# Optimization experiments

Hardware: AMD Instinct MI355X
Metric: run time of the kernel (lower is better)

## Reference

```python
import jax, jax.numpy as jnp
import numpy as np
import math

D = 512; NA = 128; NC = 256; NB = 128; BATCH = 4; H = 8
EA, EC, EB = 4, 6, 4
KA, KC, KB = 2, 1, 2
F = 4 * D  # expert_ff_mult * embed_dim
N_TOTAL = NA + NC + NB


def setup_inputs() -> dict:
    key = jax.random.key(0)
    ks = jax.random.split(key, 16)
    s = 0.02
    def nrm(k, shape, scale=s):
        return jax.random.normal(k, shape, dtype=jnp.float32) * scale
    return {
        'tokens_A': jax.random.normal(ks[0], (BATCH, NA, D), dtype=jnp.float32),
        'tokens_B': jax.random.normal(ks[1], (BATCH, NB, D), dtype=jnp.float32),
        'tokens_C': jax.random.normal(ks[2], (BATCH, NC, D), dtype=jnp.float32),
        'ln1_g': jnp.ones((3, D), jnp.float32), 'ln1_b': jnp.zeros((3, D), jnp.float32),
        'ln2_g': jnp.ones((3, D), jnp.float32), 'ln2_b': jnp.zeros((3, D), jnp.float32),
        'Wqkv': nrm(ks[3], (3 * D, D)), 'bqkv': jnp.zeros((3 * D,), jnp.float32),
        'Wo': nrm(ks[4], (D, D)), 'bo': jnp.zeros((D,), jnp.float32),
        'Wr_A': nrm(ks[5], (D, EA)), 'br_A': jnp.zeros((EA,), jnp.float32),
        'W1_A': nrm(ks[6], (EA, D, F)), 'b1_A': jnp.zeros((EA, F), jnp.float32),
        'W2_A': nrm(ks[7], (EA, F, D)), 'b2_A': jnp.zeros((EA, D), jnp.float32),
        'Wr_C': nrm(ks[8], (D, EC)), 'br_C': jnp.zeros((EC,), jnp.float32),
        'W1_C': nrm(ks[9], (EC, D, F)), 'b1_C': jnp.zeros((EC, F), jnp.float32),
        'W2_C': nrm(ks[10], (EC, F, D)), 'b2_C': jnp.zeros((EC, D), jnp.float32),
        'Wr_B': nrm(ks[11], (D, EB)), 'br_B': jnp.zeros((EB,), jnp.float32),
        'W1_B': nrm(ks[12], (EB, D, F)), 'b1_B': jnp.zeros((EB, F), jnp.float32),
        'W2_B': nrm(ks[13], (EB, F, D)), 'b2_B': jnp.zeros((EB, D), jnp.float32),
    }


def _ln(x, g, b, eps=1e-5):
    m = jnp.mean(x, axis=-1, keepdims=True)
    v = jnp.var(x, axis=-1, keepdims=True)
    return (x - m) * jax.lax.rsqrt(v + eps) * g + b


def _directed_mask_bias():
    # segments: 0=A, 1=C, 2=B in [A|C|B] order; query may attend upstream groups only
    seg = jnp.concatenate([jnp.zeros(NA), jnp.ones(NC), 2.0 * jnp.ones(NB)])
    allowed = seg[None, :] <= seg[:, None]  # (N, N)
    return jnp.where(allowed, 0.0, -1e9).astype(jnp.float32)


def _mha(x, Wqkv, bqkv, Wo, bo, mask_bias):
    B, N, _ = x.shape
    qkv = x @ Wqkv.T + bqkv  # (B, N, 3D)
    q, k, v = jnp.split(qkv, 3, axis=-1)
    hd = D // H
    def heads(t):
        return t.reshape(B, N, H, hd).transpose(0, 2, 1, 3)  # (B, H, N, hd)
    q, k, v = heads(q), heads(k), heads(v)
    scores = jnp.einsum('bhqd,bhkd->bhqk', q, k) / math.sqrt(hd) + mask_bias[None, None]
    attn = jax.nn.softmax(scores, axis=-1)
    o = jnp.einsum('bhqk,bhkd->bhqd', attn, v).transpose(0, 2, 1, 3).reshape(B, N, D)
    return o @ Wo.T + bo


def _moe(x, Wr, br, W1, b1, W2, b2, k):
    # top-k routed expert FFN: softmax gates -> top-k renormalized -> dense combine
    probs = jax.nn.softmax(x @ Wr + br, axis=-1)  # (B, N, E)
    vals, idx = jax.lax.top_k(probs, k)
    vals = vals / jnp.sum(vals, axis=-1, keepdims=True)
    E = Wr.shape[1]
    gate = jnp.sum(jax.nn.one_hot(idx, E, dtype=x.dtype) * vals[..., None], axis=-2)  # (B, N, E)
    h = jax.nn.gelu(jnp.einsum('bnd,edf->benf', x, W1) + b1[None, :, None, :])
    y = jnp.einsum('benf,efd->bend', h, W2) + b2[None, :, None, :]
    return jnp.einsum('bne,bend->bnd', gate, y)


def reference(tokens_A, tokens_B, tokens_C, ln1_g, ln1_b, ln2_g, ln2_b,
              Wqkv, bqkv, Wo, bo,
              Wr_A, br_A, W1_A, b1_A, W2_A, b2_A,
              Wr_C, br_C, W1_C, b1_C, W2_C, b2_C,
              Wr_B, br_B, W1_B, b1_B, W2_B, b2_B):
    # 1-2. group-local pre-attention LN, concat [A | C | B]
    x = jnp.concatenate([
        _ln(tokens_A, ln1_g[0], ln1_b[0]),
        _ln(tokens_C, ln1_g[1], ln1_b[1]),
        _ln(tokens_B, ln1_g[2], ln1_b[2]),
    ], axis=1)
    # 3-4. shared directed self-attention + per-group residual
    attn = _mha(x, Wqkv, bqkv, Wo, bo, _directed_mask_bias())
    tA = tokens_A + attn[:, :NA]
    tC = tokens_C + attn[:, NA:NA + NC]
    tB = tokens_B + attn[:, NA + NC:]
    # 5. group-local pre-expert LN
    nA = _ln(tA, ln2_g[0], ln2_b[0])
    nC = _ln(tC, ln2_g[1], ln2_b[1])
    nB = _ln(tB, ln2_g[2], ln2_b[2])
    # 6-9. route A and C first, then B; residual add per group
    tA = tA + _moe(nA, Wr_A, br_A, W1_A, b1_A, W2_A, b2_A, KA)
    tC = tC + _moe(nC, Wr_C, br_C, W1_C, b1_C, W2_C, b2_C, KC)
    tB = tB + _moe(nB, Wr_B, br_B, W1_B, b1_B, W2_B, b2_B, KB)
    return jnp.concatenate([tA, tC, tB], axis=1)  # (B, NA+NC+NB, D)
```

## Files before the change

### kernel.cpp

```cpp
#include <hip/hip_runtime.h>
#include <hip/hip_bf16.h>
#include <cstdint>

#define DEV __device__ __forceinline__

using f32x4  = __attribute__((ext_vector_type(4))) float;
using bf16x8 = __attribute__((ext_vector_type(8))) __bf16;

static constexpr int D_    = 512;
static constexpr int ROWS  = 2048;
static constexpr int F_    = 2048;
static constexpr int NEXP  = 14;
static constexpr int NENT  = 3072;

DEV unsigned short f2bf(float f) {
  unsigned int u = __builtin_bit_cast(unsigned int, f);
  unsigned int r = u + 0x7FFFu + ((u >> 16) & 1u);
  return (unsigned short)(r >> 16);
}
DEV unsigned int pack2(float a, float b) {
  return (unsigned int)f2bf(a) | ((unsigned int)f2bf(b) << 16);
}
DEV float gelu_tanh(float x) {
  float x3 = x * x * x;
  return 0.5f * x * (1.0f + tanhf(0.7978845608028654f * (x + 0.044715f * x3)));
}
DEV int prefix_base(const int* cnt, int e) {
  int base = 0;
  for (int i = 0; i < e; ++i) base += cnt[i];
  return base;
}

struct Shared128 { unsigned short As[128][72]; unsigned short Bs[64][72]; };

DEV void gemm128(const unsigned short* arow, const float* B, int ldb, int bcol0, int K,
                 f32x4 (&acc)[2][4], Shared128& sh)
{
  const int tid = threadIdx.x;
  const int lane = tid & 63, w = tid >> 6;
  const int ai = tid >> 1, ah = tid & 1;
  const int bj = tid >> 2, bq = tid & 3;
  for (int k0 = 0; k0 < K; k0 += 64) {
    __syncthreads();
    {
      const uint4* src = reinterpret_cast<const uint4*>(arow + k0 + ah * 32);
      uint4 v0 = src[0], v1 = src[1], v2 = src[2], v3 = src[3];
      uint4* dst = reinterpret_cast<uint4*>(&sh.As[ai][ah * 32]);
      dst[0] = v0; dst[1] = v1; dst[2] = v2; dst[3] = v3;
    }
    {
      const float4* src = reinterpret_cast<const float4*>(B + (size_t)(bcol0 + bj) * ldb + k0 + bq * 16);
      unsigned int pk[8];
      #pragma unroll
      for (int u = 0; u < 4; ++u) {
        float4 f = src[u];
        pk[u * 2]     = pack2(f.x, f.y);
        pk[u * 2 + 1] = pack2(f.z, f.w);
      }
      uint4* dst = reinterpret_cast<uint4*>(&sh.Bs[bj][bq * 16]);
      dst[0] = make_uint4(pk[0], pk[1], pk[2], pk[3]);
      dst[1] = make_uint4(pk[4], pk[5], pk[6], pk[7]);
    }
    __syncthreads();
    #pragma unroll
    for (int ks = 0; ks < 2; ++ks) {
      bf16x8 a[2], b[4];
      #pragma unroll
      for (int mi = 0; mi < 2; ++mi)
        a[mi] = *reinterpret_cast<const bf16x8*>(&sh.As[w * 32 + mi * 16 + (lane & 15)][ks * 32 + (lane >> 4) * 8]);
      #pragma unroll
      for (int ni = 0; ni < 4; ++ni)
        b[ni] = *reinterpret_cast<const bf16x8*>(&sh.Bs[ni * 16 + (lane & 15)][ks * 32 + (lane >> 4) * 8]);
      #pragma unroll
      for (int mi = 0; mi < 2; ++mi)
        #pragma unroll
        for (int ni = 0; ni < 4; ++ni)
          acc[mi][ni] = __builtin_amdgcn_mfma_f32_16x16x32_bf16(a[mi], b[ni], acc[mi][ni], 0, 0, 0);
    }
  }
}

struct Shared64x128 { unsigned short As[64][72]; unsigned short Bs[128][72]; };

DEV void gemm64x128(const unsigned short* arow, const unsigned short* B, int ldb, int bcol0, int K,
                    f32x4 (&acc)[8], Shared64x128& sh)
{
  const int tid = threadIdx.x;
  const int lane = tid & 63, w = tid >> 6;
  const int ar = tid >> 2, aq = tid & 3;
  const int br = tid >> 1, bh = tid & 1;
  for (int k0 = 0; k0 < K; k0 += 64) {
    __syncthreads();
    {
      const uint4* srcA = reinterpret_cast<const uint4*>(arow + k0 + aq * 16);
      uint4 a0 = srcA[0], a1 = srcA[1];
      uint4* dstA = reinterpret_cast<uint4*>(&sh.As[ar][aq * 16]);
      dstA[0] = a0; dstA[1] = a1;
      const uint4* srcB = reinterpret_cast<const uint4*>(B + (size_t)(bcol0 + br) * ldb + k0 + bh * 32);
      uint4 b0 = srcB[0], b1 = srcB[1], b2 = srcB[2], b3 = srcB[3];
      uint4* dstB = reinterpret_cast<uint4*>(&sh.Bs[br][bh * 32]);
      dstB[0] = b0; dstB[1] = b1; dstB[2] = b2; dstB[3] = b3;
    }
    __syncthreads();
    #pragma unroll
    for (int ks = 0; ks < 2; ++ks) {
      bf16x8 a = *reinterpret_cast<const bf16x8*>(&sh.As[w * 16 + (lane & 15)][ks * 32 + (lane >> 4) * 8]);
      #pragma unroll
      for (int ni = 0; ni < 8; ++ni) {
        bf16x8 b = *reinterpret_cast<const bf16x8*>(&sh.Bs[ni * 16 + (lane & 15)][ks * 32 + (lane >> 4) * 8]);
        acc[ni] = __builtin_amdgcn_mfma_f32_16x16x32_bf16(a, b, acc[ni], 0, 0, 0);
      }
    }
  }
}

__global__ __launch_bounds__(256) void k_ln(
    const float* tA, const float* tC, const float* tB,
    const float* g3, const float* b3, unsigned short* out)
{
  int r = blockIdx.x;
  int b = r >> 9, n = r & 511;
  int grp = n < 128 ? 0 : (n < 384 ? 1 : 2);
  const float* src = grp == 0 ? tA + (size_t)(b * 128 + n) * D_
                   : grp == 1 ? tC + (size_t)(b * 256 + n - 128) * D_
                              : tB + (size_t)(b * 128 + n - 384) * D_;
  int tid = threadIdx.x, lane = tid & 63, w = tid >> 6;
  float2 v = *reinterpret_cast<const float2*>(src + tid * 2);
  float s = v.x + v.y;
  float ss = v.x * v.x + v.y * v.y;
  #pragma unroll
  for (int off = 1; off < 64; off <<= 1) { s += __shfl_xor(s, off); ss += __shfl_xor(ss, off); }
  __shared__ float red[8];
  if (lane == 0) { red[w] = s; red[4 + w] = ss; }
  __syncthreads();
  float S  = red[0] + red[1] + red[2] + red[3];
  float SS = red[4] + red[5] + red[6] + red[7];
  float mean = S * (1.0f / 512.0f);
  float var  = SS * (1.0f / 512.0f) - mean * mean;
  float inv  = rsqrtf(var + 1e-5f);
  const float* gam = g3 + grp * D_;
  const float* bet = b3 + grp * D_;
  int d0 = tid * 2;
  out[(size_t)r * D_ + d0]     = f2bf((v.x - mean) * inv * gam[d0]     + bet[d0]);
  out[(size_t)r * D_ + d0 + 1] = f2bf((v.y - mean) * inv * gam[d0 + 1] + bet[d0 + 1]);
}

__global__ __launch_bounds__(256) void k_qkv(const unsigned short* x, const float* Wqkv, const float* bqkv,
                                             unsigned short* Qg, unsigned short* Kg, unsigned short* Vg)
{
  __shared__ Shared128 sh;
  int bn = blockIdx.x, bm = blockIdx.y, batch = blockIdx.z;
  int tid = threadIdx.x, lane = tid & 63, w = tid >> 6;
  const unsigned short* arow = x + (size_t)(batch * 512 + bm * 128 + (tid >> 1)) * D_;
  f32x4 acc[2][4] = {};
  gemm128(arow, Wqkv, 512, bn * 64, 512, acc, sh);
  #pragma unroll
  for (int mi = 0; mi < 2; ++mi)
  #pragma unroll
  for (int ni = 0; ni < 4; ++ni)
  #pragma unroll
  for (int j = 0; j < 4; ++j) {
    int n = bm * 128 + w * 32 + mi * 16 + ((lane >> 4) << 2) + j;
    int col = bn * 64 + ni * 16 + (lane & 15);
    float val = acc[mi][ni][j] + bqkv[col];
    int part = col >> 9;
    int o = col & 511, h = o >> 6, d = o & 63;
    unsigned short* dst = part == 0 ? Qg : (part == 1 ? Kg : Vg);
    dst[(size_t)((batch * 8 + h) * 512 + n) * 64 + d] = f2bf(val);
  }
}

__global__ __launch_bounds__(64) void k_attn(const unsigned short* Qg, const unsigned short* Kg,
                                             const unsigned short* Vg, unsigned short* attn)
{
  __shared__ unsigned short Qs[16][72], Ks[64][72], VT[64][72], Ps[16][72];
  int qt16 = blockIdx.x, h = blockIdx.y, b = blockIdx.z;
  int lane = threadIdx.x;
  const unsigned short* Qb  = Qg + (size_t)((b * 8 + h) * 512) * 64;
  const unsigned short* Kbp = Kg + (size_t)((b * 8 + h) * 512) * 64;
  const unsigned short* Vbp = Vg + (size_t)((b * 8 + h) * 512) * 64;
  int q0 = qt16 * 16;
  {
    int row = lane >> 2, q4 = lane & 3;
    const uint4* src = reinterpret_cast<const uint4*>(Qb + (size_t)(q0 + row) * 64 + q4 * 16);
    uint4* dst = reinterpret_cast<uint4*>(&Qs[row][q4 * 16]);
    dst[0] = src[0]; dst[1] = src[1];
  }
  int nkt = qt16 < 8 ? 2 : (qt16 < 24 ? 6 : 8);
  float mrun[4] = { -1e30f, -1e30f, -1e30f, -1e30f };
  float lrun[4] = {};
  f32x4 o[4] = {};
  for (int kt = 0; kt < nkt; ++kt) {
    #pragma unroll
    for (int it = 0; it < 4; ++it) {
      int row = it * 16 + (lane >> 2), q4 = lane & 3;
      const uint4* ksrc = reinterpret_cast<const uint4*>(Kbp + (size_t)(kt * 64 + row) * 64 + q4 * 16);
      uint4* kdst = reinterpret_cast<uint4*>(&Ks[row][q4 * 16]);
      kdst[0] = ksrc[0]; kdst[1] = ksrc[1];
      union { uint4 u; unsigned short s[8]; } vv0, vv1;
      const uint4* vsrc = reinterpret_cast<const uint4*>(Vbp + (size_t)(kt * 64 + row) * 64 + q4 * 16);
      vv0.u = vsrc[0]; vv1.u = vsrc[1];
      #pragma unroll
      for (int jj = 0; jj < 8; ++jj) {
        VT[q4 * 16 + jj][row]     = vv0.s[jj];
        VT[q4 * 16 + 8 + jj][row] = vv1.s[jj];
      }
    }
    f32x4 s[4] = {};
    #pragma unroll
    for (int ks = 0; ks < 2; ++ks) {
      bf16x8 aq = *reinterpret_cast<const bf16x8*>(&Qs[lane & 15][ks * 32 + (lane >> 4) * 8]);
      #pragma unroll
      for (int cc = 0; cc < 4; ++cc) {
        bf16x8 bk = *reinterpret_cast<const bf16x8*>(&Ks[cc * 16 + (lane & 15)][ks * 32 + (lane >> 4) * 8]);
        s[cc] = __builtin_amdgcn_mfma_f32_16x16x32_bf16(aq, bk, s[cc], 0, 0, 0);
      }
    }
    #pragma unroll
    for (int rr = 0; rr < 4; ++rr) {
      float s0 = s[0][rr] * 0.125f, s1 = s[1][rr] * 0.125f;
      float s2 = s[2][rr] * 0.125f, s3 = s[3][rr] * 0.125f;
      float mx = fmaxf(fmaxf(s0, s1), fmaxf(s2, s3));
      #pragma unroll
      for (int off = 1; off < 16; off <<= 1) mx = fmaxf(mx, __shfl_xor(mx, off));
      float mn = fmaxf(mrun[rr], mx);
      float al = expf(mrun[rr] - mn);
      mrun[rr] = mn;
      float p0 = expf(s0 - mn), p1 = expf(s1 - mn), p2 = expf(s2 - mn), p3 = expf(s3 - mn);
      float ps = p0 + p1 + p2 + p3;
      #pragma unroll
      for (int off = 1; off < 16; off <<= 1) ps += __shfl_xor(ps, off);
      lrun[rr] = lrun[rr] * al + ps;
      #pragma unroll
      for (int n4 = 0; n4 < 4; ++n4) o[n4][rr] *= al;
      int prow = ((lane >> 4) << 2) + rr;
      Ps[prow][0 * 16 + (lane & 15)] = f2bf(p0);
      Ps[prow][1 * 16 + (lane & 15)] = f2bf(p1);
      Ps[prow][2 * 16 + (lane & 15)] = f2bf(p2);
      Ps[prow][3 * 16 + (lane & 15)] = f2bf(p3);
    }
    #pragma unroll
    for (int ks = 0; ks < 2; ++ks) {
      bf16x8 ap = *reinterpret_cast<const bf16x8*>(&Ps[lane & 15][ks * 32 + (lane >> 4) * 8]);
      #pragma unroll
      for (int n4 = 0; n4 < 4; ++n4) {
        bf16x8 bv = *reinterpret_cast<const bf16x8*>(&VT[n4 * 16 + (lane & 15)][ks * 32 + (lane >> 4) * 8]);
        o[n4] = __builtin_amdgcn_mfma_f32_16x16x32_bf16(ap, bv, o[n4], 0, 0, 0);
      }
    }
  }
  #pragma unroll
  for (int n4 = 0; n4 < 4; ++n4)
  #pragma unroll
  for (int rr = 0; rr < 4; ++rr) {
    int qrow = q0 + ((lane >> 4) << 2) + rr;
    int col = h * 64 + n4 * 16 + (lane & 15);
    float val = o[n4][rr] / lrun[rr];
    attn[(size_t)(b * 512 + qrow) * 512 + col] = f2bf(val);
  }
}

__global__ __launch_bounds__(256) void k_wo(const unsigned short* attn, const float* Wo, const float* bo,
                                            const float* tokA, const float* tokC, const float* tokB,
                                            float* out)
{
  __shared__ Shared128 sh;
  int bn = blockIdx.x, bm = blockIdx.y;
  int tid = threadIdx.x, lane = tid & 63, w = tid >> 6;
  const unsigned short* arow = attn + (size_t)(bm * 128 + (tid >> 1)) * D_;
  f32x4 acc[2][4] = {};
  gemm128(arow, Wo, 512, bn * 64, 512, acc, sh);
  #pragma unroll
  for (int mi = 0; mi < 2; ++mi)
  #pragma unroll
  for (int ni = 0; ni < 4; ++ni)
  #pragma unroll
  for (int j = 0; j < 4; ++j) {
    int row = bm * 128 + w * 32 + mi * 16 + ((lane >> 4) << 2) + j;
    int col = bn * 64 + ni * 16 + (lane & 15);
    float val = acc[mi][ni][j] + bo[col];
    int b = row >> 9, n = row & 511;
    float res;
    if (n < 128)      res = tokA[(size_t)(b * 128 + n) * D_ + col];
    else if (n < 384) res = tokC[(size_t)(b * 256 + n - 128) * D_ + col];
    else              res = tokB[(size_t)(b * 128 + n - 384) * D_ + col];
    out[(size_t)row * D_ + col] = res + val;
  }
}

__global__ __launch_bounds__(256) void k_router(const float* t,
    const float* ln2g, const float* ln2b,
    const float* WrA, const float* brA, const float* WrC, const float* brC,
    const float* WrB, const float* brB,
    int* cnt, int* tokexp, float* tokgate, unsigned short* nrm)
{
  int w = threadIdx.x >> 6, lane = threadIdx.x & 63;
  int r = blockIdx.x * 4 + w;
  int n = r & 511;
  int grp = n < 128 ? 0 : (n < 384 ? 1 : 2);
  int E = grp == 1 ? 6 : 4;
  int topk = grp == 1 ? 1 : 2;
  int egbase = grp == 0 ? 0 : (grp == 1 ? 4 : 10);
  const float* Wr = grp == 0 ? WrA : (grp == 1 ? WrC : WrB);
  const float* br = grp == 0 ? brA : (grp == 1 ? brC : brB);
  const float* tr = t + (size_t)r * D_;
  float xv[8];
  float s = 0.0f, ss = 0.0f;
  #pragma unroll
  for (int it = 0; it < 8; ++it) {
    float v = tr[it * 64 + lane];
    xv[it] = v; s += v; ss += v * v;
  }
  #pragma unroll
  for (int off = 1; off < 64; off <<= 1) { s += __shfl_xor(s, off); ss += __shfl_xor(ss, off); }
  float mean = s * (1.0f / 512.0f);
  float var  = ss * (1.0f / 512.0f) - mean * mean;
  float inv  = rsqrtf(var + 1e-5f);
  const float* gam = ln2g + grp * D_;
  const float* bet = ln2b + grp * D_;
  float acc[6] = {};
  #pragma unroll
  for (int it = 0; it < 8; ++it) {
    int d = it * 64 + lane;
    float nv = (xv[it] - mean) * inv * gam[d] + bet[d];
    nrm[(size_t)r * D_ + d] = f2bf(nv);
    #pragma unroll
    for (int e = 0; e < 6; ++e) if (e < E) acc[e] += nv * Wr[d * E + e];
  }
  #pragma unroll
  for (int e = 0; e < 6; ++e)
    #pragma unroll
    for (int off = 1; off < 64; off <<= 1) acc[e] += __shfl_xor(acc[e], off);
  if (lane == 0) {
    float p[6];
    float mx = -1e30f;
    #pragma unroll
    for (int e = 0; e < 6; ++e) if (e < E) { p[e] = acc[e] + br[e]; mx = fmaxf(mx, p[e]); }
    float sum = 0.0f;
    #pragma unroll
    for (int e = 0; e < 6; ++e) if (e < E) { p[e] = expf(p[e] - mx); sum += p[e]; }
    #pragma unroll
    for (int e = 0; e < 6; ++e) if (e < E) p[e] /= sum;
    int i1 = 0; float v1 = p[0];
    #pragma unroll
    for (int e = 1; e < 6; ++e) if (e < E && p[e] > v1) { v1 = p[e]; i1 = e; }
    if (topk == 1) {
      tokexp[r * 2]     = egbase + i1; tokgate[r * 2]     = 1.0f;
      tokexp[r * 2 + 1] = -1;          tokgate[r * 2 + 1] = 0.0f;
      atomicAdd(&cnt[egbase + i1], 1);
    } else {
      int i2 = -1; float v2 = -1e30f;
      #pragma unroll
      for (int e = 0; e < 6; ++e) if (e < E && e != i1 && p[e] > v2) { v2 = p[e]; i2 = e; }
      float tot = v1 + v2;
      tokexp[r * 2]     = egbase + i1; tokgate[r * 2]     = v1 / tot;
      tokexp[r * 2 + 1] = egbase + i2; tokgate[r * 2 + 1] = v2 / tot;
      atomicAdd(&cnt[egbase + i1], 1);
      atomicAdd(&cnt[egbase + i2], 1);
    }
  }
}

__global__ __launch_bounds__(256) void k_scatter(const int* tokexp, const float* tokgate,
                                                 const int* cnt, int* cursor, int* list, float* gate)
{
  int r = blockIdx.x * 256 + threadIdx.x;
  #pragma unroll
  for (int j = 0; j < 2; ++j) {
    int e = tokexp[r * 2 + j];
    if (e >= 0) {
      int base = prefix_base(cnt, e);
      int s = atomicAdd(&cursor[e], 1);
      list[base + s] = r;
      gate[base + s] = tokgate[r * 2 + j];
    }
  }
}

__global__ __launch_bounds__(256) void k_trAll(
    const float* w1A, const float* w1C, const float* w1B,
    const float* w2A, const float* w2C, const float* w2B,
    unsigned short* W1T, unsigned short* W2T)
{
  int bx = blockIdx.x, by = blockIdx.y, z = blockIdx.z;
  const float* src;
  unsigned short* dst;
  int ldS, ldD, R0, C0;
  if (z < 14) {
    int e = z;
    src = e < 4 ? w1A + (size_t)e * D_ * F_ : e < 10 ? w1C + (size_t)(e - 4) * D_ * F_ : w1B + (size_t)(e - 10) * D_ * F_;
    dst = W1T + (size_t)e * F_ * D_;
    ldS = F_; ldD = D_;
    R0 = by * 64;
    C0 = bx * 64;
  } else {
    int e = z - 14;
    src = e < 4 ? w2A + (size_t)e * F_ * D_ : e < 10 ? w2C + (size_t)(e - 4) * F_ * D_ : w2B + (size_t)(e - 10) * F_ * D_;
    dst = W2T + (size_t)e * D_ * F_;
    ldS = D_; ldD = F_;
    R0 = bx * 64;
    C0 = by * 64;
  }
  __shared__ float tile[64][65];
  int t = threadIdx.x, r = t >> 2, q = t & 3;
  const float4* sp = reinterpret_cast<const float4*>(src + (size_t)(R0 + r) * ldS + C0 + q * 16);
  #pragma unroll
  for (int u = 0; u < 4; ++u) {
    float4 v = sp[u];
    tile[r][q * 16 + u * 4 + 0] = v.x; tile[r][q * 16 + u * 4 + 1] = v.y;
    tile[r][q * 16 + u * 4 + 2] = v.z; tile[r][q * 16 + u * 4 + 3] = v.w;
  }
  __syncthreads();
  int c = t >> 2;
  unsigned int pk[8];
  #pragma unroll
  for (int i = 0; i < 8; ++i) {
    float fa = tile[q * 16 + 2 * i][c];
    float fb = tile[q * 16 + 2 * i + 1][c];
    pk[i] = pack2(fa, fb);
  }
  uint4* dp = reinterpret_cast<uint4*>(dst + (size_t)(C0 + c) * ldD + R0 + q * 16);
  dp[0] = make_uint4(pk[0], pk[1], pk[2], pk[3]);
  dp[1] = make_uint4(pk[4], pk[5], pk[6], pk[7]);
}

__global__ __launch_bounds__(256) void k_moe1(const unsigned short* nrm, const unsigned short* W1T,
    const float* b1A, const float* b1C, const float* b1B,
    const int* cnt, const int* list, unsigned short* H)
{
  int ft = blockIdx.x, tt = blockIdx.y, e = blockIdx.z;
  int c = cnt[e];
  if (tt * 64 >= c) return;
  __shared__ Shared64x128 sh;
  const float* b1 = e < 4 ? b1A + (size_t)e * F_ : e < 10 ? b1C + (size_t)(e - 4) * F_ : b1B + (size_t)(e - 10) * F_;
  const unsigned short* Wt = W1T + (size_t)e * F_ * D_;
  int base = prefix_base(cnt, e);
  int tid = threadIdx.x, lane = tid & 63, w = tid >> 6;
  int ig = tt * 64 + (tid >> 2);
  int tok = list[base + (ig < c ? ig : c - 1)];
  const unsigned short* arow = nrm + (size_t)tok * D_;
  f32x4 acc[8] = {};
  gemm64x128(arow, Wt, 512, ft * 128, 512, acc, sh);
  #pragma unroll
  for (int ni = 0; ni < 8; ++ni)
  #pragma unroll
  for (int j = 0; j < 4; ++j) {
    int rl = w * 16 + ((lane >> 4) << 2) + j;
    int sg = tt * 64 + rl;
    if (sg < c) {
      int col = ft * 128 + ni * 16 + (lane & 15);
      float val = acc[ni][j] + b1[col];
      H[(size_t)(base + sg) * F_ + col] = f2bf(gelu_tanh(val));
    }
  }
}

__global__ __launch_bounds__(256) void k_moe2(const unsigned short* H, const unsigned short* W2T,
    const float* b2A, const float* b2C, const float* b2B,
    const int* cnt, const int* list, const float* gate, float* out)
{
  int dt = blockIdx.x, tt = blockIdx.y >> 2, kc = blockIdx.y & 3, e = blockIdx.z;
  int c = cnt[e];
  if (tt * 64 >= c) return;
  __shared__ Shared64x128 sh;
  const float* b2 = e < 4 ? b2A + (size_t)e * D_ : e < 10 ? b2C + (size_t)(e - 4) * D_ : b2B + (size_t)(e - 10) * D_;
  const unsigned short* Wt = W2T + (size_t)e * D_ * F_ + kc * 512;
  int base = prefix_base(cnt, e);
  int tid = threadIdx.x, lane = tid & 63, w = tid >> 6;
  int ig = tt * 64 + (tid >> 2);
  const unsigned short* arow = H + (size_t)(base + (ig < c ? ig : c - 1)) * F_ + kc * 512;
  f32x4 acc[8] = {};
  gemm64x128(arow, Wt, F_, dt * 128, 512, acc, sh);
  #pragma unroll
  for (int ni = 0; ni < 8; ++ni)
  #pragma unroll
  for (int j = 0; j < 4; ++j) {
    int rl = w * 16 + ((lane >> 4) << 2) + j;
    int sg = tt * 64 + rl;
    if (sg < c) {
      int col = dt * 128 + ni * 16 + (lane & 15);
      float val = acc[ni][j] + (kc == 0 ? b2[col] : 0.0f);
      int tok = list[base + sg];
      atomicAdd(&out[(size_t)tok * D_ + col], gate[base + sg] * val);
    }
  }
}

extern "C" void kernel_launch(void* const* d_in, const int* in_sizes, int n_in,
                              void* d_out, int out_size, void* d_ws, size_t ws_size,
                              hipStream_t stream)
{
  const float* tokA = (const float*)d_in[0];
  const float* tokB = (const float*)d_in[1];
  const float* tokC = (const float*)d_in[2];
  const float* ln1g = (const float*)d_in[3];
  const float* ln1b = (const float*)d_in[4];
  const float* ln2g = (const float*)d_in[5];
  const float* ln2b = (const float*)d_in[6];
  const float* Wqkv = (const float*)d_in[7];
  const float* bqkv = (const float*)d_in[8];
  const float* Wo   = (const float*)d_in[9];
  const float* bo   = (const float*)d_in[10];
  const float* WrA  = (const float*)d_in[11];
  const float* brA  = (const float*)d_in[12];
  const float* W1A  = (const float*)d_in[13];
  const float* b1A  = (const float*)d_in[14];
  const float* W2A  = (const float*)d_in[15];
  const float* b2A  = (const float*)d_in[16];
  const float* WrC  = (const float*)d_in[17];
  const float* brC  = (const float*)d_in[18];
  const float* W1C  = (const float*)d_in[19];
  const float* b1C  = (const float*)d_in[20];
  const float* W2C  = (const float*)d_in[21];
  const float* b2C  = (const float*)d_in[22];
  const float* WrB  = (const float*)d_in[23];
  const float* brB  = (const float*)d_in[24];
  const float* W1B  = (const float*)d_in[25];
  const float* b1B  = (const float*)d_in[26];
  const float* W2B  = (const float*)d_in[27];
  const float* b2B  = (const float*)d_in[28];
  float* out = (float*)d_out;

  char* ws = (char*)d_ws;
  const size_t MB = 1024 * 1024;
  const size_t WSTRIDE = (size_t)NEXP * F_ * D_ * 2;
  unsigned short* xb   = (unsigned short*)(ws);
  unsigned short* nrm  = xb;
  unsigned short* Qg   = (unsigned short*)(ws + 2 * MB);
  unsigned short* Kg   = (unsigned short*)(ws + 4 * MB);
  unsigned short* Vg   = (unsigned short*)(ws + 6 * MB);
  unsigned short* attn = (unsigned short*)(ws + 8 * MB);
  unsigned short* W1T  = (unsigned short*)(ws + 16 * MB);
  unsigned short* W2T  = (unsigned short*)(ws + 16 * MB + WSTRIDE);
  unsigned short* H    = (unsigned short*)(ws + 16 * MB + 2 * WSTRIDE);
  char* small = ws + 16 * MB + 2 * WSTRIDE + (size_t)NENT * F_ * 2;
  int*   cnt     = (int*)(small);
  int*   cursor  = (int*)(small + 64);
  int*   tokexp  = (int*)(small + 256);
  float* tokgate = (float*)(small + 256 + ROWS * 2 * 4);
  int*   list    = (int*)(small + 256 + ROWS * 4 * 4);
  float* gate    = (float*)(small + 256 + ROWS * 4 * 4 + NENT * 4);

  hipMemsetAsync(cnt, 0, 128, stream);
  k_ln<<<ROWS, 256, 0, stream>>>(tokA, tokC, tokB, ln1g, ln1b, xb);
  k_qkv<<<dim3(24, 4, 4), 256, 0, stream>>>(xb, Wqkv, bqkv, Qg, Kg, Vg);
  k_attn<<<dim3(32, 8, 4), 64, 0, stream>>>(Qg, Kg, Vg, attn);
  k_wo<<<dim3(8, 16), 256, 0, stream>>>(attn, Wo, bo, tokA, tokC, tokB, out);
  k_router<<<512, 256, 0, stream>>>(out, ln2g, ln2b, WrA, brA, WrC, brC, WrB, brB,
                                    cnt, tokexp, tokgate, nrm);
  k_scatter<<<8, 256, 0, stream>>>(tokexp, tokgate, cnt, cursor, list, gate);
  k_trAll<<<dim3(32, 8, 28), 256, 0, stream>>>(W1A, W1C, W1B, W2A, W2C, W2B, W1T, W2T);
  k_moe1<<<dim3(16, 16, 14), 256, 0, stream>>>(nrm, W1T, b1A, b1C, b1B, cnt, list, H);
  k_moe2<<<dim3(4, 64, 14), 256, 0, stream>>>(H, W2T, b2A, b2C, b2B, cnt, list, gate, out);
}
```

Measured before the change: 230.2 us.

## Prepack expert weights into MFMA fragment order and load B directly to registers

The weight transpose kernel is replaced by a pack kernel that converts expert weights to bf16 and lays them out in per-tile MFMA fragment order. The MoE GEMMs then load B fragments straight from global memory into registers with coalesced 16-byte loads, which removes the B shared-memory staging and its LDS traffic. Only A is still staged in shared memory. In exchange, each wave holds 16 fragment registers per k-tile, and all four waves load the same B fragments redundantly, relying on cache for reuse.

```diff
diff --git a/kernel.cpp b/kernel.cpp
--- a/kernel.cpp
+++ b/kernel.cpp
@@ -80,37 +80,35 @@
   }
 }
 
-struct Shared64x128 { unsigned short As[64][72]; unsigned short Bs[128][72]; };
-
-DEV void gemm64x128(const unsigned short* arow, const unsigned short* B, int ldb, int bcol0, int K,
-                    f32x4 (&acc)[8], Shared64x128& sh)
+DEV void gemm64x128p(const unsigned short* arow, const unsigned short* Bt,
+                     f32x4 (&acc)[8], unsigned short (&As)[64][72])
 {
   const int tid = threadIdx.x;
   const int lane = tid & 63, w = tid >> 6;
   const int ar = tid >> 2, aq = tid & 3;
-  const int br = tid >> 1, bh = tid & 1;
-  for (int k0 = 0; k0 < K; k0 += 64) {
+  #pragma unroll
+  for (int kt = 0; kt < 8; ++kt) {
+    bf16x8 b[16];
+    const unsigned short* bb = Bt + kt * 8192 + lane * 8;
+    #pragma unroll
+    for (int f = 0; f < 16; ++f)
+      b[f] = *reinterpret_cast<const bf16x8*>(bb + f * 512);
     __syncthreads();
     {
-      const uint4* srcA = reinterpret_cast<const uint4*>(arow + k0 + aq * 16);
+      const uint4* srcA = reinterpret_cast<const uint4*>(arow + kt * 64 + aq * 16);
       uint4 a0 = srcA[0], a1 = srcA[1];
-      uint4* dstA = reinterpret_cast<uint4*>(&sh.As[ar][aq * 16]);
+      uint4* dstA = reinterpret_cast<uint4*>(&As[ar][aq * 16]);
       dstA[0] = a0; dstA[1] = a1;
-      const uint4* srcB = reinterpret_cast<const uint4*>(B + (size_t)(bcol0 + br) * ldb + k0 + bh * 32);
-      uint4 b0 = srcB[0], b1 = srcB[1], b2 = srcB[2], b3 = srcB[3];
-      uint4* dstB = reinterpret_cast<uint4*>(&sh.Bs[br][bh * 32]);
-      dstB[0] = b0; dstB[1] = b1; dstB[2] = b2; dstB[3] = b3;
     }
     __syncthreads();
-    #pragma unroll
-    for (int ks = 0; ks < 2; ++ks) {
-      bf16x8 a = *reinterpret_cast<const bf16x8*>(&sh.As[w * 16 + (lane & 15)][ks * 32 + (lane >> 4) * 8]);
-      #pragma unroll
-      for (int ni = 0; ni < 8; ++ni) {
-        bf16x8 b = *reinterpret_cast<const bf16x8*>(&sh.Bs[ni * 16 + (lane & 15)][ks * 32 + (lane >> 4) * 8]);
-        acc[ni] = __builtin_amdgcn_mfma_f32_16x16x32_bf16(a, b, acc[ni], 0, 0, 0);
-      }
-    }
+    bf16x8 a0 = *reinterpret_cast<const bf16x8*>(&As[w * 16 + (lane & 15)][0 * 32 + (lane >> 4) * 8]);
+    bf16x8 a1 = *reinterpret_cast<const bf16x8*>(&As[w * 16 + (lane & 15)][1 * 32 + (lane >> 4) * 8]);
+    #pragma unroll
+    for (int ni = 0; ni < 8; ++ni)
+      acc[ni] = __builtin_amdgcn_mfma_f32_16x16x32_bf16(a0, b[ni * 2 + 0], acc[ni], 0, 0, 0);
+    #pragma unroll
+    for (int ni = 0; ni < 8; ++ni)
+      acc[ni] = __builtin_amdgcn_mfma_f32_16x16x32_bf16(a1, b[ni * 2 + 1], acc[ni], 0, 0, 0);
   }
 }
 
@@ -377,70 +375,75 @@
   }
 }
 
-__global__ __launch_bounds__(256) void k_trAll(
+__global__ __launch_bounds__(256) void k_pack(
     const float* w1A, const float* w1C, const float* w1B,
     const float* w2A, const float* w2C, const float* w2B,
-    unsigned short* W1T, unsigned short* W2T)
-{
-  int bx = blockIdx.x, by = blockIdx.y, z = blockIdx.z;
+    unsigned short* W1P, unsigned short* W2P)
+{
+  int bx = blockIdx.x, z = blockIdx.y;
   const float* src;
-  unsigned short* dst;
-  int ldS, ldD, R0, C0;
+  unsigned short* dstbase;
+  int ld, ntile, ktile, KT;
   if (z < 14) {
     int e = z;
     src = e < 4 ? w1A + (size_t)e * D_ * F_ : e < 10 ? w1C + (size_t)(e - 4) * D_ * F_ : w1B + (size_t)(e - 10) * D_ * F_;
-    dst = W1T + (size_t)e * F_ * D_;
-    ldS = F_; ldD = D_;
-    R0 = by * 64;
-    C0 = bx * 64;
+    dstbase = W1P + (size_t)e * F_ * D_;
+    ld = F_; KT = 8;
+    ntile = bx >> 3; ktile = bx & 7;
   } else {
     int e = z - 14;
     src = e < 4 ? w2A + (size_t)e * F_ * D_ : e < 10 ? w2C + (size_t)(e - 4) * F_ * D_ : w2B + (size_t)(e - 10) * F_ * D_;
-    dst = W2T + (size_t)e * D_ * F_;
-    ldS = D_; ldD = F_;
-    R0 = bx * 64;
-    C0 = by * 64;
-  }
-  __shared__ float tile[64][65];
-  int t = threadIdx.x, r = t >> 2, q = t & 3;
-  const float4* sp = reinterpret_cast<const float4*>(src + (size_t)(R0 + r) * ldS + C0 + q * 16);
-  #pragma unroll
-  for (int u = 0; u < 4; ++u) {
-    float4 v = sp[u];
-    tile[r][q * 16 + u * 4 + 0] = v.x; tile[r][q * 16 + u * 4 + 1] = v.y;
-    tile[r][q * 16 + u * 4 + 2] = v.z; tile[r][q * 16 + u * 4 + 3] = v.w;
+    dstbase = W2P + (size_t)e * D_ * F_;
+    ld = D_; KT = 32;
+    ntile = bx >> 5; ktile = bx & 31;
+  }
+  int k0 = ktile * 64, n0 = ntile * 128;
+  __shared__ unsigned short sh[64][138];
+  int t = threadIdx.x;
+  {
+    int r = t >> 2, q = t & 3;
+    const float4* sp = reinterpret_cast<const float4*>(src + (size_t)(k0 + r) * ld + n0 + q * 32);
+    unsigned int* shw = reinterpret_cast<unsigned int*>(&sh[r][q * 32]);
+    #pragma unroll
+    for (int u = 0; u < 8; ++u) {
+      float4 v = sp[u];
+      shw[u * 2]     = pack2(v.x, v.y);
+      shw[u * 2 + 1] = pack2(v.z, v.w);
+    }
   }
   __syncthreads();
-  int c = t >> 2;
-  unsigned int pk[8];
-  #pragma unroll
-  for (int i = 0; i < 8; ++i) {
-    float fa = tile[q * 16 + 2 * i][c];
-    float fb = tile[q * 16 + 2 * i + 1][c];
-    pk[i] = pack2(fa, fb);
-  }
-  uint4* dp = reinterpret_cast<uint4*>(dst + (size_t)(C0 + c) * ldD + R0 + q * 16);
-  dp[0] = make_uint4(pk[0], pk[1], pk[2], pk[3]);
-  dp[1] = make_uint4(pk[4], pk[5], pk[6], pk[7]);
-}
-
-__global__ __launch_bounds__(256) void k_moe1(const unsigned short* nrm, const unsigned short* W1T,
+  size_t tbase = (size_t)(ntile * KT + ktile) * 8192;
+  #pragma unroll
+  for (int i = 0; i < 4; ++i) {
+    int p = t + 256 * i;
+    int f = p >> 6, l = p & 63;
+    int ks = f & 1, ni = f >> 1;
+    int nl = ni * 16 + (l & 15);
+    int kl = ks * 32 + (l >> 4) * 8;
+    unsigned short tmp[8];
+    #pragma unroll
+    for (int j = 0; j < 8; ++j) tmp[j] = sh[kl + j][nl];
+    *reinterpret_cast<uint4*>(dstbase + tbase + (size_t)p * 8) = *reinterpret_cast<const uint4*>(tmp);
+  }
+}
+
+__global__ __launch_bounds__(256) void k_moe1(const unsigned short* nrm, const unsigned short* W1P,
     const float* b1A, const float* b1C, const float* b1B,
     const int* cnt, const int* list, unsigned short* H)
 {
   int ft = blockIdx.x, tt = blockIdx.y, e = blockIdx.z;
   int c = cnt[e];
   if (tt * 64 >= c) return;
-  __shared__ Shared64x128 sh;
+  __shared__ unsigned short As[64][72];
   const float* b1 = e < 4 ? b1A + (size_t)e * F_ : e < 10 ? b1C + (size_t)(e - 4) * F_ : b1B + (size_t)(e - 10) * F_;
-  const unsigned short* Wt = W1T + (size_t)e * F_ * D_;
+  const unsigned short* Bt = W1P + (size_t)e * F_ * D_ + (size_t)(ft * 8) * 8192;
   int base = prefix_base(cnt, e);
   int tid = threadIdx.x, lane = tid & 63, w = tid >> 6;
   int ig = tt * 64 + (tid >> 2);
   int tok = list[base + (ig < c ? ig : c - 1)];
   const unsigned short* arow = nrm + (size_t)tok * D_;
   f32x4 acc[8] = {};
-  gemm64x128(arow, Wt, 512, ft * 128, 512, acc, sh);
+  gemm64x128p(arow, Bt, acc, As);
   #pragma unroll
   for (int ni = 0; ni < 8; ++ni)
   #pragma unroll
@@ -455,22 +458,22 @@
   }
 }
 
-__global__ __launch_bounds__(256) void k_moe2(const unsigned short* H, const unsigned short* W2T,
+__global__ __launch_bounds__(256) void k_moe2(const unsigned short* H, const unsigned short* W2P,
     const float* b2A, const float* b2C, const float* b2B,
     const int* cnt, const int* list, const float* gate, float* out)
 {
   int dt = blockIdx.x, tt = blockIdx.y >> 2, kc = blockIdx.y & 3, e = blockIdx.z;
   int c = cnt[e];
   if (tt * 64 >= c) return;
-  __shared__ Shared64x128 sh;
+  __shared__ unsigned short As[64][72];
   const float* b2 = e < 4 ? b2A + (size_t)e * D_ : e < 10 ? b2C + (size_t)(e - 4) * D_ : b2B + (size_t)(e - 10) * D_;
-  const unsigned short* Wt = W2T + (size_t)e * D_ * F_ + kc * 512;
+  const unsigned short* Bt = W2P + (size_t)e * D_ * F_ + (size_t)(dt * 32 + kc * 8) * 8192;
   int base = prefix_base(cnt, e);
   int tid = threadIdx.x, lane = tid & 63, w = tid >> 6;
   int ig = tt * 64 + (tid >> 2);
   const unsigned short* arow = H + (size_t)(base + (ig < c ? ig : c - 1)) * F_ + kc * 512;
   f32x4 acc[8] = {};
-  gemm64x128(arow, Wt, F_, dt * 128, 512, acc, sh);
+  gemm64x128p(arow, Bt, acc, As);
   #pragma unroll
   for (int ni = 0; ni < 8; ++ni)
   #pragma unroll
@@ -530,8 +533,8 @@
   unsigned short* Kg   = (unsigned short*)(ws + 4 * MB);
   unsigned short* Vg   = (unsigned short*)(ws + 6 * MB);
   unsigned short* attn = (unsigned short*)(ws + 8 * MB);
-  unsigned short* W1T  = (unsigned short*)(ws + 16 * MB);
-  unsigned short* W2T  = (unsigned short*)(ws + 16 * MB + WSTRIDE);
+  unsigned short* W1P  = (unsigned short*)(ws + 16 * MB);
+  unsigned short* W2P  = (unsigned short*)(ws + 16 * MB + WSTRIDE);
   unsigned short* H    = (unsigned short*)(ws + 16 * MB + 2 * WSTRIDE);
   char* small = ws + 16 * MB + 2 * WSTRIDE + (size_t)NENT * F_ * 2;
   int*   cnt     = (int*)(small);
@@ -549,7 +552,7 @@
   k_router<<<512, 256, 0, stream>>>(out, ln2g, ln2b, WrA, brA, WrC, brC, WrB, brB,
                                     cnt, tokexp, tokgate, nrm);
   k_scatter<<<8, 256, 0, stream>>>(tokexp, tokgate, cnt, cursor, list, gate);
-  k_trAll<<<dim3(32, 8, 28), 256, 0, stream>>>(W1A, W1C, W1B, W2A, W2C, W2B, W1T, W2T);
-  k_moe1<<<dim3(16, 16, 14), 256, 0, stream>>>(nrm, W1T, b1A, b1C, b1B, cnt, list, H);
-  k_moe2<<<dim3(4, 64, 14), 256, 0, stream>>>(H, W2T, b2A, b2C, b2B, cnt, list, gate, out);
-}
+  k_pack<<<dim3(128, 28), 256, 0, stream>>>(W1A, W1C, W1B, W2A, W2C, W2B, W1P, W2P);
+  k_moe1<<<dim3(16, 16, 14), 256, 0, stream>>>(nrm, W1P, b1A, b1C, b1B, cnt, list, H);
+  k_moe2<<<dim3(4, 64, 14), 256, 0, stream>>>(H, W2P, b2A, b2C, b2B, cnt, list, gate, out);
+}
```

After: 246.0 us. 1.07x slower.
